# Optimization experiments

Measured on AMD Instinct MI355X. Metric: run time of the kernel, lower is better.

## Reference

```python
import jax, jax.numpy as jnp
import numpy as np
from jax import lax

B, T, DIN, D = 8, 4096, 1024, 256
H, DK, DV, DFF, P = 8, 32, 32, 1024, 4
KC, NS = 64, 4
SCALES = jnp.array([16.0, 64.0, 128.0, 256.0], dtype=jnp.float32)
K = KC * NS


def _pos_embedding(rel, d_model):
    # rel: [B,K,2] normalized (start,end) -> sinusoidal emb [B,K,d_model]
    d4 = d_model // 4
    freq = jnp.exp(-jnp.log(10000.0) * jnp.arange(d4, dtype=jnp.float32) / d4)
    ang = rel[..., None] * freq                                  # [B,K,2,d4]
    emb = jnp.concatenate([jnp.sin(ang), jnp.cos(ang)], axis=-1) # [B,K,2,2*d4]
    return emb.reshape(rel.shape[0], rel.shape[1], d_model)


def _pool(feat, s, e):
    # ROI pooling by P linearly spaced samples in [s,e); feat [B,T,D], s/e [B,K]
    frac = (jnp.arange(P, dtype=jnp.float32) + 0.5) / P
    idx = jnp.clip(jnp.floor(s[..., None] + (e - s)[..., None] * frac), 0, T - 1).astype(jnp.int32)
    b, k = idx.shape[0], idx.shape[1]
    out = jnp.take_along_axis(feat, idx.reshape(b, k * P)[..., None], axis=1)  # [B,K*P,D]
    return out.reshape(b, k, P, feat.shape[-1])


def _ln(x, g, b):
    m = x.mean(-1, keepdims=True)
    v = ((x - m) ** 2).mean(-1, keepdims=True)
    return (x - m) * lax.rsqrt(v + 1e-6) * g + b


def setup_inputs():
    ks = jax.random.split(jax.random.key(0), 16)
    n = lambda i, sh, s=0.02: jax.random.normal(ks[i], sh, jnp.float32) * s
    return dict(
        feature=jax.random.normal(ks[0], (B, T, DIN), jnp.float32),
        pos_ind=jnp.tile(jnp.arange(T, dtype=jnp.int32)[None], (B, 1)),
        feature_mask=jnp.ones((B, T), jnp.float32),
        W_red=n(1, (DIN, D)), b_red=jnp.zeros((D,), jnp.float32),
        conv1_w=n(2, (D, D, 3)), conv1_b=jnp.zeros((D,), jnp.float32),
        conv2_w=n(3, (D, D, 3)), conv2_b=jnp.zeros((D,), jnp.float32),
        W_sc=n(4, (D, 3)), b_sc=jnp.zeros((3,), jnp.float32),
        W_pool=n(5, (3 * P * D, D)), b_pool=jnp.zeros((D,), jnp.float32),
        Wq=n(6, (D, H * DK)), Wk=n(7, (D, H * DK)), Wv=n(8, (D, H * DV)),
        Wo=n(9, (H * DV, D)),
        ln1_g=jnp.ones((D,), jnp.float32), ln1_b=jnp.zeros((D,), jnp.float32),
        W1=n(10, (D, DFF)), b1=jnp.zeros((DFF,), jnp.float32),
        W2=n(11, (DFF, D)), b2=jnp.zeros((D,), jnp.float32),
        ln2_g=jnp.ones((D,), jnp.float32), ln2_b=jnp.zeros((D,), jnp.float32),
        W_cls=n(12, (D, 2)), b_cls=jnp.zeros((2,), jnp.float32),
    )


def _forward(feature, feature_mask, W_red, b_red, conv1_w, conv1_b, conv2_w, conv2_b,
             W_sc, b_sc, W_pool, b_pool, Wq, Wk, Wv, Wo, ln1_g, ln1_b,
             W1, b1, W2, b2, ln2_g, ln2_b, W_cls, b_cls):
    enc_input = jax.nn.selu(feature @ W_red + b_red)            # [B,T,D]
    h = enc_input.transpose(0, 2, 1)                            # [B,D,T]
    dn = ('NCH', 'OIH', 'NCH')
    h = jax.nn.relu(lax.conv_general_dilated(h, conv1_w, (1,), [(1, 1)], dimension_numbers=dn) + conv1_b[None, :, None])
    h = jax.nn.relu(lax.conv_general_dilated(h, conv2_w, (1,), [(1, 1)], dimension_numbers=dn) + conv2_b[None, :, None])
    enc_output = h.transpose(0, 2, 1)                           # [B,T,D]
    score_output = jax.nn.sigmoid(enc_output @ W_sc + b_sc)     # [B,T,3]

    # --- proposal_layer (fixed-size, jit-safe): top-KC actness peaks x NS scales ---
    actness = score_output[..., 0] * feature_mask               # [B,T]
    topv, topi = lax.top_k(actness, KC)                         # [B,KC]
    c = topi.astype(jnp.float32)[:, :, None]                    # [B,KC,1]
    half = SCALES[None, None, :] / 2.0
    s = jnp.clip(c - half, 0.0, T - 1.0).reshape(B, K)
    e = jnp.clip(c + half, 1.0, float(T)).reshape(B, K)
    e = jnp.maximum(e, s + 1.0)
    L = e - s
    ss, se = jnp.clip(s - L / 4, 0.0, T - 1.0), s + L / 4       # start region
    es, ee = e - L / 4, jnp.clip(e + L / 4, 1.0, float(T))      # end region
    rois_mask = jnp.broadcast_to((topv > 0.5)[:, :, None], (B, KC, NS)).reshape(B, K).astype(jnp.float32)
    roi_actness = jnp.broadcast_to(topv[:, :, None], (B, KC, NS)).reshape(B, K)
    rel = jnp.stack([s / T, e / T], axis=-1)                    # [B,K,2]
    pos_emb = _pos_embedding(rel, D)                            # [B,K,D]

    # --- ROI_Relation: pool(start/mid/end) -> fc -> MHSA + FFN (post-LN) ---
    pooled = jnp.concatenate([_pool(enc_input, ss, se), _pool(enc_input, s, e), _pool(enc_input, es, ee)], axis=2)
    x0 = pooled.reshape(B, K, 3 * P * D) @ W_pool + b_pool + pos_emb  # [B,K,D]
    q = (x0 @ Wq).reshape(B, K, H, DK)
    kk = (x0 @ Wk).reshape(B, K, H, DK)
    v = (x0 @ Wv).reshape(B, K, H, DV)
    att = jnp.einsum('bqhd,bkhd->bhqk', q, kk) / np.sqrt(DK).astype(np.float32)
    att = att + (1.0 - rois_mask)[:, None, None, :] * -1e9
    ctx = jnp.einsum('bhqk,bkhd->bqhd', jax.nn.softmax(att, axis=-1), v).reshape(B, K, H * DV)
    x1 = _ln(x0 + ctx @ Wo, ln1_g, ln1_b)
    x2 = _ln(x1 + jax.nn.relu(x1 @ W1 + b1) @ W2 + b2, ln2_g, ln2_b)
    roi_scores = jax.nn.softmax(x2 @ W_cls + b_cls, axis=2)     # [B,K,2]
    rois_se = jnp.stack([s, e], axis=-1)                        # rois[:, :, 1:]
    return rois_se, roi_actness, roi_scores


def reference(feature, pos_ind, feature_mask, W_red, b_red, conv1_w, conv1_b, conv2_w, conv2_b, W_sc, b_sc, W_pool, b_pool, Wq, Wk, Wv, Wo, ln1_g, ln1_b, W1, b1, W2, b2, ln2_g, ln2_b, W_cls, b_cls):
    del pos_ind  # carried through pipeline but unused in this forward
    return _forward(feature, feature_mask, W_red, b_red, conv1_w, conv1_b, conv2_w, conv2_b, W_sc, b_sc, W_pool, b_pool, Wq, Wk, Wv, Wo, ln1_g, ln1_b, W1, b1, W2, b2, ln2_g, ln2_b, W_cls, b_cls)
```

## Files before the change

kernel.cpp:

```cpp
#include <hip/hip_runtime.h>
#include <hip/hip_bf16.h>
#include <math.h>

#define NB 8
#define NT 4096
#define NBT 32768
#define NDIN 1024
#define ND 256
#define NH 8
#define NDK 32
#define NKC 64
#define NNS 4
#define NRK 256
#define NROI 2048

#define F4Z make_float4(0.f, 0.f, 0.f, 0.f)

__global__ __launch_bounds__(256) void transw_k(const float* __restrict__ w1,
    const float* __restrict__ w2, float* __restrict__ Wt1, float* __restrict__ Wt2)
{
  int i = blockIdx.x * 256 + threadIdx.x;
  const float* w = (i >= 196608) ? w2 : w1;
  float* Wt = (i >= 196608) ? Wt2 : Wt1;
  int j = (i >= 196608) ? (i - 196608) : i;
  int co = j & 255;
  int rest = j >> 8;
  int ci = rest & 255;
  int tap = rest >> 8;
  Wt[j] = w[(size_t)co * 768 + ci * 3 + tap];
}

__global__ __launch_bounds__(256) void concatw_k(const float* __restrict__ Wq,
    const float* __restrict__ Wk, const float* __restrict__ Wv,
    float* __restrict__ Wqkv)
{
  int d = blockIdx.x * 256 + threadIdx.x;
  int r = d / 768, c = d % 768;
  int m = c >> 8, cc = c & 255;
  const float* src = (m == 0) ? Wq : (m == 1) ? Wk : Wv;
  Wqkv[d] = src[r * 256 + cc];
}

__global__ __launch_bounds__(256) void gemm1_k(const float* __restrict__ A,
    const float* __restrict__ W, const float* __restrict__ bias,
    float* __restrict__ C, int M, int Ka, int N)
{
  __shared__ float As[16][132];
  __shared__ float Ws[16][128];
  int tid = threadIdx.x;
  int tx = tid & 15, ty = tid >> 4;
  int m0 = blockIdx.x * 128, n0 = blockIdx.y * 128;
  int ar = tid >> 1, acg = tid & 1;
  int wk = tid >> 5, wn = tid & 31;
  float4 pa0, pa1, pw0, pw1;

#define G1LOAD(kk) do { \
    pa0 = *reinterpret_cast<const float4*>(A + (size_t)(m0 + ar) * Ka + (kk) + (acg * 2 + 0) * 4); \
    pa1 = *reinterpret_cast<const float4*>(A + (size_t)(m0 + ar) * Ka + (kk) + (acg * 2 + 1) * 4); \
    pw0 = *reinterpret_cast<const float4*>(W + (size_t)((kk) + wk) * N + n0 + wn * 4); \
    pw1 = *reinterpret_cast<const float4*>(W + (size_t)((kk) + 8 + wk) * N + n0 + wn * 4); \
  } while (0)
#define G1WRITE() do { \
    int cg0 = acg * 2, cg1 = acg * 2 + 1; \
    As[cg0 * 4 + 0][ar] = pa0.x; As[cg0 * 4 + 1][ar] = pa0.y; \
    As[cg0 * 4 + 2][ar] = pa0.z; As[cg0 * 4 + 3][ar] = pa0.w; \
    As[cg1 * 4 + 0][ar] = pa1.x; As[cg1 * 4 + 1][ar] = pa1.y; \
    As[cg1 * 4 + 2][ar] = pa1.z; As[cg1 * 4 + 3][ar] = pa1.w; \
    *reinterpret_cast<float4*>(&Ws[wk][wn * 4]) = pw0; \
    *reinterpret_cast<float4*>(&Ws[8 + wk][wn * 4]) = pw1; \
  } while (0)

  int NC = Ka >> 4;
  float acc[8][8] = {};
  G1LOAD(0);
  G1WRITE();
  __syncthreads();
  for (int c = 0; c < NC; ++c) {
    if (c + 1 < NC) G1LOAD((c + 1) * 16);
#pragma unroll
    for (int k = 0; k < 16; ++k) {
      float4 xa = *reinterpret_cast<const float4*>(&As[k][ty * 4]);
      float4 xb = *reinterpret_cast<const float4*>(&As[k][64 + ty * 4]);
      float4 wa = *reinterpret_cast<const float4*>(&Ws[k][tx * 4]);
      float4 wb = *reinterpret_cast<const float4*>(&Ws[k][64 + tx * 4]);
      float aa[8] = {xa.x, xa.y, xa.z, xa.w, xb.x, xb.y, xb.z, xb.w};
      float bb[8] = {wa.x, wa.y, wa.z, wa.w, wb.x, wb.y, wb.z, wb.w};
#pragma unroll
      for (int i = 0; i < 8; ++i)
#pragma unroll
        for (int j = 0; j < 8; ++j)
          acc[i][j] += aa[i] * bb[j];
    }
    __syncthreads();
    if (c + 1 < NC) {
      G1WRITE();
      __syncthreads();
    }
  }
#undef G1LOAD
#undef G1WRITE
#pragma unroll
  for (int i = 0; i < 8; ++i) {
    int row = m0 + ((i < 4) ? (ty * 4 + i) : (64 + ty * 4 + (i - 4)));
#pragma unroll
    for (int jh = 0; jh < 2; ++jh) {
      int col = n0 + jh * 64 + tx * 4;
      float o[4];
#pragma unroll
      for (int j = 0; j < 4; ++j) {
        float v = acc[i][jh * 4 + j] + bias[col + j];
        v = (v > 0.f) ? 1.0507009873554805f * v
                      : 1.0507009873554805f * 1.6732632423543772f * expm1f(v);
        o[j] = v;
      }
      *reinterpret_cast<float4*>(C + (size_t)row * N + col) =
          make_float4(o[0], o[1], o[2], o[3]);
    }
  }
}

template<int EPI>
__global__ __launch_bounds__(256) void conv_t(const float* __restrict__ in,
    const float* __restrict__ Wt, const float* __restrict__ bias,
    float* __restrict__ out, const float* __restrict__ Wsc,
    float* __restrict__ pscore)
{
  __shared__ float As[16][132];
  __shared__ float Ws[16][128];
  int tid = threadIdx.x;
  int tx = tid & 15, ty = tid >> 4;
  int m0 = blockIdx.x * 128, n0 = blockIdx.y * 128;
  int bstart = m0 & ~(NT - 1);
  int ar = tid >> 1, acg = tid & 1;
  int wk = tid >> 5, wn = tid & 31;
  float4 pa0, pa1, pw0, pw1;

#define CLOAD(kk) do { \
    int tap = (kk) >> 8, kd = (kk) & 255; \
    int g = m0 - 1 + tap + ar; \
    bool ok = (g >= bstart) && (g < bstart + NT); \
    pa0 = ok ? *reinterpret_cast<const float4*>(in + (size_t)g * 256 + kd + (acg * 2 + 0) * 4) : F4Z; \
    pa1 = ok ? *reinterpret_cast<const float4*>(in + (size_t)g * 256 + kd + (acg * 2 + 1) * 4) : F4Z; \
    pw0 = *reinterpret_cast<const float4*>(Wt + (size_t)((kk) + wk) * 256 + n0 + wn * 4); \
    pw1 = *reinterpret_cast<const float4*>(Wt + (size_t)((kk) + 8 + wk) * 256 + n0 + wn * 4); \
  } while (0)
#define CWRITE() do { \
    int cg0 = acg * 2, cg1 = acg * 2 + 1; \
    As[cg0 * 4 + 0][ar] = pa0.x; As[cg0 * 4 + 1][ar] = pa0.y; \
    As[cg0 * 4 + 2][ar] = pa0.z; As[cg0 * 4 + 3][ar] = pa0.w; \
    As[cg1 * 4 + 0][ar] = pa1.x; As[cg1 * 4 + 1][ar] = pa1.y; \
    As[cg1 * 4 + 2][ar] = pa1.z; As[cg1 * 4 + 3][ar] = pa1.w; \
    *reinterpret_cast<float4*>(&Ws[wk][wn * 4]) = pw0; \
    *reinterpret_cast<float4*>(&Ws[8 + wk][wn * 4]) = pw1; \
  } while (0)

  float acc[8][8] = {};
  CLOAD(0);
  CWRITE();
  __syncthreads();
  for (int c = 0; c < 48; ++c) {
    if (c + 1 < 48) CLOAD((c + 1) * 16);
#pragma unroll
    for (int k = 0; k < 16; ++k) {
      float4 xa = *reinterpret_cast<const float4*>(&As[k][ty * 4]);
      float4 xb = *reinterpret_cast<const float4*>(&As[k][64 + ty * 4]);
      float4 wa = *reinterpret_cast<const float4*>(&Ws[k][tx * 4]);
      float4 wb = *reinterpret_cast<const float4*>(&Ws[k][64 + tx * 4]);
      float aa[8] = {xa.x, xa.y, xa.z, xa.w, xb.x, xb.y, xb.z, xb.w};
      float bb[8] = {wa.x, wa.y, wa.z, wa.w, wb.x, wb.y, wb.z, wb.w};
#pragma unroll
      for (int i = 0; i < 8; ++i)
#pragma unroll
        for (int j = 0; j < 8; ++j)
          acc[i][j] += aa[i] * bb[j];
    }
    __syncthreads();
    if (c + 1 < 48) {
      CWRITE();
      __syncthreads();
    }
  }
#undef CLOAD
#undef CWRITE

  if (EPI == 0) {
#pragma unroll
    for (int i = 0; i < 8; ++i) {
      int row = m0 + ((i < 4) ? (ty * 4 + i) : (64 + ty * 4 + (i - 4)));
#pragma unroll
      for (int jh = 0; jh < 2; ++jh) {
        int col = n0 + jh * 64 + tx * 4;
        float o[4];
#pragma unroll
        for (int j = 0; j < 4; ++j)
          o[j] = fmaxf(acc[i][jh * 4 + j] + bias[col + j], 0.f);
        *reinterpret_cast<float4*>(out + (size_t)row * 256 + col) =
            make_float4(o[0], o[1], o[2], o[3]);
      }
    }
  } else {
    float p[8];
#pragma unroll
    for (int i = 0; i < 8; ++i) {
      float s = 0.f;
#pragma unroll
      for (int jh = 0; jh < 2; ++jh)
#pragma unroll
        for (int j = 0; j < 4; ++j) {
          int col = n0 + jh * 64 + tx * 4 + j;
          float v = fmaxf(acc[i][jh * 4 + j] + bias[col], 0.f);
          s += v * Wsc[col * 3];
        }
      p[i] = s;
    }
#pragma unroll
    for (int off = 1; off < 16; off <<= 1)
#pragma unroll
      for (int i = 0; i < 8; ++i)
        p[i] += __shfl_xor(p[i], off, 64);
    if (tx == 0) {
#pragma unroll
      for (int i = 0; i < 8; ++i) {
        int row = m0 + ((i < 4) ? (ty * 4 + i) : (64 + ty * 4 + (i - 4)));
        pscore[(size_t)row * 2 + blockIdx.y] = p[i];
      }
    }
  }
}

__global__ __launch_bounds__(256) void actness_k(const float* __restrict__ pscore,
    const float* __restrict__ bsc, const float* __restrict__ fmask,
    float* __restrict__ actness)
{
  int g = blockIdx.x * 256 + threadIdx.x;
  float2 pv = *reinterpret_cast<const float2*>(pscore + (size_t)g * 2);
  float z = pv.x + pv.y + bsc[0];
  actness[g] = (1.f / (1.f + expf(-z))) * fmask[g];
}

template<int ACT>
__global__ __launch_bounds__(256) void gemm_k(const float* __restrict__ A,
    const float* __restrict__ W, const float* __restrict__ bias,
    const float* __restrict__ resid, float* __restrict__ C,
    int M, int Ka, int N)
{
  __shared__ float As[16][66];
  __shared__ float Ws[16][68];
  int tid = threadIdx.x;
  int tx = tid & 15, ty = tid >> 4;
  int m0 = blockIdx.x * 64, n0 = blockIdx.y * 64;
  int lr = tid >> 2, lc = tid & 3;
  int wr = tid >> 4, wc = tid & 15;
  float4 pav, pwv;
  int NC = Ka >> 4;

#define GLOAD(kk) do { \
    pav = *reinterpret_cast<const float4*>(A + (size_t)(m0 + lr) * Ka + (kk) + lc * 4); \
    pwv = *reinterpret_cast<const float4*>(W + (size_t)((kk) + wr) * N + n0 + wc * 4); \
  } while (0)
#define GWRITE() do { \
    As[lc * 4 + 0][lr] = pav.x; As[lc * 4 + 1][lr] = pav.y; \
    As[lc * 4 + 2][lr] = pav.z; As[lc * 4 + 3][lr] = pav.w; \
    *reinterpret_cast<float4*>(&Ws[wr][wc * 4]) = pwv; \
  } while (0)

  float acc[4][4] = {};
  GLOAD(0);
  GWRITE();
  __syncthreads();
  for (int c = 0; c < NC; ++c) {
    if (c + 1 < NC) GLOAD((c + 1) * 16);
#pragma unroll
    for (int k = 0; k < 16; ++k) {
      float4 a4 = *reinterpret_cast<const float4*>(&As[k][ty * 4]);
      float4 b4 = *reinterpret_cast<const float4*>(&Ws[k][tx * 4]);
      float aa[4] = {a4.x, a4.y, a4.z, a4.w};
      float bb[4] = {b4.x, b4.y, b4.z, b4.w};
#pragma unroll
      for (int i = 0; i < 4; ++i)
#pragma unroll
        for (int j = 0; j < 4; ++j)
          acc[i][j] += aa[i] * bb[j];
    }
    __syncthreads();
    if (c + 1 < NC) {
      GWRITE();
      __syncthreads();
    }
  }
#undef GLOAD
#undef GWRITE
#pragma unroll
  for (int i = 0; i < 4; ++i) {
    int row = m0 + ty * 4 + i;
    float o[4];
#pragma unroll
    for (int j = 0; j < 4; ++j) {
      int col = n0 + tx * 4 + j;
      float v = acc[i][j];
      if (bias) v += bias[col];
      if (resid) v += resid[(size_t)row * N + col];
      if (ACT == 1) {
        v = (v > 0.f) ? 1.0507009873554805f * v
                      : 1.0507009873554805f * 1.6732632423543772f * expm1f(v);
      } else if (ACT == 2) {
        v = fmaxf(v, 0.f);
      }
      o[j] = v;
    }
    *reinterpret_cast<float4*>(C + (size_t)row * N + n0 + tx * 4) =
        make_float4(o[0], o[1], o[2], o[3]);
  }
}

__global__ __launch_bounds__(256) void topk_k(const float* __restrict__ actness,
    float* __restrict__ topv, int* __restrict__ topi)
{
  __shared__ float wbv[4];
  __shared__ int wbi[4];
  __shared__ float gbv;
  __shared__ int gbi;
  int b = blockIdx.x;
  int tid = threadIdx.x;
  int lane = tid & 63, wvi = tid >> 6;
  float v[16];
  const float* src = actness + (size_t)b * NT + tid * 16;
#pragma unroll
  for (int j = 0; j < 16; j += 4)
    *reinterpret_cast<float4*>(&v[j]) = *reinterpret_cast<const float4*>(src + j);
  for (int it = 0; it < NKC; ++it) {
    float best = -1e30f; int bj = 0;
#pragma unroll
    for (int j = 0; j < 16; ++j)
      if (v[j] > best) { best = v[j]; bj = j; }
    int bidx = tid * 16 + bj;
#pragma unroll
    for (int off = 1; off < 64; off <<= 1) {
      float ov = __shfl_xor(best, off, 64);
      int oi = __shfl_xor(bidx, off, 64);
      if (ov > best || (ov == best && oi < bidx)) { best = ov; bidx = oi; }
    }
    if (lane == 0) { wbv[wvi] = best; wbi[wvi] = bidx; }
    __syncthreads();
    if (tid == 0) {
      float bb = wbv[0]; int bi2 = wbi[0];
#pragma unroll
      for (int w = 1; w < 4; ++w)
        if (wbv[w] > bb || (wbv[w] == bb && wbi[w] < bi2)) { bb = wbv[w]; bi2 = wbi[w]; }
      topv[b * NKC + it] = bb;
      topi[b * NKC + it] = bi2;
      gbv = bb; gbi = bi2;
    }
    __syncthreads();
    int gi = gbi;
    if ((gi >> 4) == tid) v[gi & 15] = -1e30f;
  }
}

__global__ __launch_bounds__(256) void rois_k(const float* __restrict__ topv,
    const int* __restrict__ topi, int* __restrict__ idxb, float* __restrict__ rmask,
    float* __restrict__ rel, float* __restrict__ out_rois, float* __restrict__ out_act)
{
  int t = blockIdx.x * 256 + threadIdx.x;
  if (t >= NROI) return;
  int b = t >> 8, k = t & 255, kc = k >> 2, ns = k & 3;
  float tv = topv[b * NKC + kc];
  float c = (float)topi[b * NKC + kc];
  const float scales[4] = {16.f, 64.f, 128.f, 256.f};
  float half = scales[ns] * 0.5f;
  float s = fminf(fmaxf(c - half, 0.f), 4095.f);
  float e = fminf(fmaxf(c + half, 1.f), 4096.f);
  e = fmaxf(e, s + 1.f);
  float L = e - s;
  float ss = fminf(fmaxf(s - L * 0.25f, 0.f), 4095.f);
  float se = s + L * 0.25f;
  float es = e - L * 0.25f;
  float ee = fminf(fmaxf(e + L * 0.25f, 1.f), 4096.f);
  float st[3] = {ss, s, es};
  float en[3] = {se, e, ee};
#pragma unroll
  for (int r = 0; r < 3; ++r)
#pragma unroll
    for (int p = 0; p < 4; ++p) {
      float frac = ((float)p + 0.5f) * 0.25f;
      float fidx = floorf(st[r] + (en[r] - st[r]) * frac);
      fidx = fminf(fmaxf(fidx, 0.f), 4095.f);
      idxb[t * 12 + r * 4 + p] = (int)fidx;
    }
  rmask[t] = (tv > 0.5f) ? 1.f : 0.f;
  rel[t * 2 + 0] = s * (1.f / 4096.f);
  rel[t * 2 + 1] = e * (1.f / 4096.f);
  out_rois[t * 2 + 0] = s;
  out_rois[t * 2 + 1] = e;
  out_act[t] = tv;
}

__global__ __launch_bounds__(256) void pool_gemm_k(const float* __restrict__ enc,
    const int* __restrict__ idxb, const float* __restrict__ Wp,
    const float* __restrict__ bp, const float* __restrict__ rel,
    float* __restrict__ x0)
{
  __shared__ float As[16][66];
  __shared__ float Ws[16][68];
  int tid = threadIdx.x;
  int tx = tid & 15, ty = tid >> 4;
  int m0 = blockIdx.x * 64, n0 = blockIdx.y * 64;
  int lr = tid >> 2, lc = tid & 3;
  int wr = tid >> 4, wc = tid & 15;
  int roi = m0 + lr;
  int b = roi >> 8;
  float4 pav, pwv;

#define PLOAD(kk) do { \
    int slot = (kk) >> 8, kd = (kk) & 255; \
    int trow = idxb[roi * 12 + slot]; \
    pav = *reinterpret_cast<const float4*>(enc + ((size_t)(b * NT + trow)) * 256 + kd + lc * 4); \
    pwv = *reinterpret_cast<const float4*>(Wp + (size_t)((kk) + wr) * 256 + n0 + wc * 4); \
  } while (0)
#define PWRITE() do { \
    As[lc * 4 + 0][lr] = pav.x; As[lc * 4 + 1][lr] = pav.y; \
    As[lc * 4 + 2][lr] = pav.z; As[lc * 4 + 3][lr] = pav.w; \
    *reinterpret_cast<float4*>(&Ws[wr][wc * 4]) = pwv; \
  } while (0)

  float acc[4][4] = {};
  PLOAD(0);
  PWRITE();
  __syncthreads();
  for (int c = 0; c < 192; ++c) {
    if (c + 1 < 192) PLOAD((c + 1) * 16);
#pragma unroll
    for (int k = 0; k < 16; ++k) {
      float4 a4 = *reinterpret_cast<const float4*>(&As[k][ty * 4]);
      float4 b4 = *reinterpret_cast<const float4*>(&Ws[k][tx * 4]);
      float aa[4] = {a4.x, a4.y, a4.z, a4.w};
      float bb[4] = {b4.x, b4.y, b4.z, b4.w};
#pragma unroll
      for (int i = 0; i < 4; ++i)
#pragma unroll
        for (int j = 0; j < 4; ++j)
          acc[i][j] += aa[i] * bb[j];
    }
    __syncthreads();
    if (c + 1 < 192) {
      PWRITE();
      __syncthreads();
    }
  }
#undef PLOAD
#undef PWRITE
#pragma unroll
  for (int i = 0; i < 4; ++i) {
    int rr = m0 + ty * 4 + i;
    float r0 = rel[rr * 2], r1 = rel[rr * 2 + 1];
    float o[4];
#pragma unroll
    for (int j = 0; j < 4; ++j) {
      int col = n0 + tx * 4 + j;
      int rsel = col >> 7, cc = col & 127, j2 = cc & 63;
      float freq = expf(-0.14391156831212787f * (float)j2);
      float ang = ((rsel == 0) ? r0 : r1) * freq;
      float pe = (cc < 64) ? sinf(ang) : cosf(ang);
      o[j] = acc[i][j] + bp[col] + pe;
    }
    *reinterpret_cast<float4*>(x0 + (size_t)rr * 256 + n0 + tx * 4) =
        make_float4(o[0], o[1], o[2], o[3]);
  }
}

__global__ __launch_bounds__(256) void attn_k(const float* __restrict__ qkv,
    const float* __restrict__ rmask, float* __restrict__ ctx)
{
  __shared__ float ks[256][32];
  __shared__ float vs[256][32];
  int bh = blockIdx.x;
  int b = bh >> 3, h = bh & 7;
  int tid = threadIdx.x;
  size_t rowb = (size_t)b * 256;
  for (int idx = tid; idx < 2048; idx += 256) {
    int r = idx >> 3, dg = idx & 7;
    *reinterpret_cast<float4*>(&ks[r][dg * 4]) =
        *reinterpret_cast<const float4*>(qkv + (rowb + r) * 768 + 256 + h * 32 + dg * 4);
    *reinterpret_cast<float4*>(&vs[r][dg * 4]) =
        *reinterpret_cast<const float4*>(qkv + (rowb + r) * 768 + 512 + h * 32 + dg * 4);
  }
  __syncthreads();
  float qr[32];
#pragma unroll
  for (int dg = 0; dg < 8; ++dg)
    *reinterpret_cast<float4*>(&qr[dg * 4]) =
        *reinterpret_cast<const float4*>(qkv + (rowb + tid) * 768 + h * 32 + dg * 4);
  const float invs = 0.17677669529663689f;
  float m = -1e30f, l = 0.f;
  float accd[32] = {};
  for (int kk = 0; kk < 256; ++kk) {
    float s = 0.f;
#pragma unroll
    for (int d = 0; d < 32; ++d) s += qr[d] * ks[kk][d];
    s = s * invs + (1.f - rmask[b * 256 + kk]) * -1e9f;
    if (s > m) {
      float corr = expf(m - s);
      l *= corr;
#pragma unroll
      for (int d = 0; d < 32; ++d) accd[d] *= corr;
      m = s;
    }
    float p = expf(s - m);
    l += p;
#pragma unroll
    for (int d = 0; d < 32; ++d) accd[d] += p * vs[kk][d];
  }
  float inv = 1.f / l;
#pragma unroll
  for (int dg = 0; dg < 8; ++dg) {
    float4 o = make_float4(accd[dg * 4] * inv, accd[dg * 4 + 1] * inv,
                           accd[dg * 4 + 2] * inv, accd[dg * 4 + 3] * inv);
    *reinterpret_cast<float4*>(ctx + (rowb + tid) * 256 + h * 32 + dg * 4) = o;
  }
}

__global__ __launch_bounds__(256) void ln_k(float* __restrict__ x,
    const float* __restrict__ g, const float* __restrict__ bb)
{
  int row = blockIdx.x * 4 + (threadIdx.x >> 6);
  int lane = threadIdx.x & 63;
  float* xr = x + (size_t)row * 256;
  float4 v = *reinterpret_cast<const float4*>(xr + lane * 4);
  float s = v.x + v.y + v.z + v.w;
#pragma unroll
  for (int off = 32; off > 0; off >>= 1) s += __shfl_xor(s, off, 64);
  float mean = s * 0.00390625f;
  float dx[4] = {v.x - mean, v.y - mean, v.z - mean, v.w - mean};
  float s2 = dx[0] * dx[0] + dx[1] * dx[1] + dx[2] * dx[2] + dx[3] * dx[3];
#pragma unroll
  for (int off = 32; off > 0; off >>= 1) s2 += __shfl_xor(s2, off, 64);
  float var = s2 * 0.00390625f;
  float rs = 1.f / sqrtf(var + 1e-6f);
  int c = lane * 4;
  float4 o;
  o.x = dx[0] * rs * g[c + 0] + bb[c + 0];
  o.y = dx[1] * rs * g[c + 1] + bb[c + 1];
  o.z = dx[2] * rs * g[c + 2] + bb[c + 2];
  o.w = dx[3] * rs * g[c + 3] + bb[c + 3];
  *reinterpret_cast<float4*>(xr + lane * 4) = o;
}

__global__ __launch_bounds__(256) void cls_k(const float* __restrict__ x2,
    const float* __restrict__ Wc, const float* __restrict__ bc,
    float* __restrict__ out)
{
  int row = blockIdx.x * 4 + (threadIdx.x >> 6);
  int lane = threadIdx.x & 63;
  const float* xr = x2 + (size_t)row * 256;
  float4 xv = *reinterpret_cast<const float4*>(xr + lane * 4);
  int c = lane * 4;
  float4 w01 = *reinterpret_cast<const float4*>(Wc + c * 2);
  float4 w23 = *reinterpret_cast<const float4*>(Wc + c * 2 + 4);
  float l0 = xv.x * w01.x + xv.y * w01.z + xv.z * w23.x + xv.w * w23.z;
  float l1 = xv.x * w01.y + xv.y * w01.w + xv.z * w23.y + xv.w * w23.w;
#pragma unroll
  for (int off = 32; off > 0; off >>= 1) {
    l0 += __shfl_xor(l0, off, 64);
    l1 += __shfl_xor(l1, off, 64);
  }
  if (lane == 0) {
    l0 += bc[0]; l1 += bc[1];
    float mm = fmaxf(l0, l1);
    float e0 = expf(l0 - mm), e1 = expf(l1 - mm);
    float inv = 1.f / (e0 + e1);
    out[row * 2 + 0] = e0 * inv;
    out[row * 2 + 1] = e1 * inv;
  }
}

extern "C" void kernel_launch(void* const* d_in, const int* in_sizes, int n_in,
                              void* d_out, int out_size, void* d_ws, size_t ws_size,
                              hipStream_t stream) {
  (void)in_sizes; (void)n_in; (void)out_size; (void)ws_size;
  const float* feature = (const float*)d_in[0];
  const float* fmask   = (const float*)d_in[2];
  const float* W_red   = (const float*)d_in[3];
  const float* b_red   = (const float*)d_in[4];
  const float* conv1_w = (const float*)d_in[5];
  const float* conv1_b = (const float*)d_in[6];
  const float* conv2_w = (const float*)d_in[7];
  const float* conv2_b = (const float*)d_in[8];
  const float* W_sc    = (const float*)d_in[9];
  const float* b_sc    = (const float*)d_in[10];
  const float* W_pool  = (const float*)d_in[11];
  const float* b_pool  = (const float*)d_in[12];
  const float* Wq      = (const float*)d_in[13];
  const float* Wk      = (const float*)d_in[14];
  const float* Wv      = (const float*)d_in[15];
  const float* Wo      = (const float*)d_in[16];
  const float* ln1_g   = (const float*)d_in[17];
  const float* ln1_b   = (const float*)d_in[18];
  const float* W1      = (const float*)d_in[19];
  const float* b1      = (const float*)d_in[20];
  const float* W2      = (const float*)d_in[21];
  const float* b2      = (const float*)d_in[22];
  const float* ln2_g   = (const float*)d_in[23];
  const float* ln2_b   = (const float*)d_in[24];
  const float* W_cls   = (const float*)d_in[25];
  const float* b_cls   = (const float*)d_in[26];

  float* ws = (float*)d_ws;
  float* enc   = ws;
  float* h1    = ws + 8388608;
  float* Wt1   = ws + 16777216;
  float* Wt2   = ws + 16973824;
  float* act   = ws + 17170432;
  float* topv  = ws + 17203200;
  int*   topi  = (int*)(ws + 17203712);
  int*   idxb  = (int*)(ws + 17204224);
  float* rmask = ws + 17228800;
  float* rel   = ws + 17230848;
  float* pscore = ws + 17234944;
  float* x0   = h1;
  float* qkv  = h1 + 524288;
  float* ctx  = h1 + 2097152;
  float* x1   = h1 + 2621440;
  float* ft   = h1 + 3145728;
  float* x2   = h1 + 5242880;
  float* Wqkv = h1 + 5767168;

  float* orois  = (float*)d_out;
  float* oact   = orois + 4096;
  float* oscore = orois + 6144;

  transw_k<<<1536, 256, 0, stream>>>(conv1_w, conv2_w, Wt1, Wt2);
  gemm1_k<<<dim3(256, 2), 256, 0, stream>>>(feature, W_red, b_red, enc,
                                            NBT, NDIN, ND);
  conv_t<0><<<dim3(256, 2), 256, 0, stream>>>(enc, Wt1, conv1_b, h1, nullptr, nullptr);
  conv_t<1><<<dim3(256, 2), 256, 0, stream>>>(h1, Wt2, conv2_b, nullptr, W_sc, pscore);
  actness_k<<<128, 256, 0, stream>>>(pscore, b_sc, fmask, act);
  topk_k<<<NB, 256, 0, stream>>>(act, topv, topi);
  rois_k<<<NB, 256, 0, stream>>>(topv, topi, idxb, rmask, rel, orois, oact);
  concatw_k<<<768, 256, 0, stream>>>(Wq, Wk, Wv, Wqkv);
  pool_gemm_k<<<dim3(32, 4), 256, 0, stream>>>(enc, idxb, W_pool, b_pool, rel, x0);
  gemm_k<0><<<dim3(32, 12), 256, 0, stream>>>(x0, Wqkv, nullptr, nullptr, qkv,
                                              NROI, ND, 768);
  attn_k<<<NB * NH, 256, 0, stream>>>(qkv, rmask, ctx);
  gemm_k<0><<<dim3(32, 4), 256, 0, stream>>>(ctx, Wo, nullptr, x0, x1, NROI, ND, ND);
  ln_k<<<512, 256, 0, stream>>>(x1, ln1_g, ln1_b);
  gemm_k<2><<<dim3(32, 16), 256, 0, stream>>>(x1, W1, b1, nullptr, ft, NROI, ND, 1024);
  gemm_k<0><<<dim3(32, 4), 256, 0, stream>>>(ft, W2, b2, x1, x2, NROI, 1024, ND);
  ln_k<<<512, 256, 0, stream>>>(x2, ln2_g, ln2_b);
  cls_k<<<512, 256, 0, stream>>>(x2, W_cls, b_cls, oscore);
}
```

Measured before the change: 1.197 ms.

## Enlarge GEMM/conv tiles to 256 rows with 512 threads; drop prefetch in small GEMMs

The main GEMM and both conv kernels now use 512-thread blocks covering 256 rows by 128 columns, so each weight tile staged in shared memory serves twice as many rows and the grid is halved. Each thread still computes an 8x8 output fragment. Separately, the small gemm_k and pool_gemm_k kernels drop their register prefetch double-buffering in favour of a simpler load-sync-compute loop, which lowers register pressure but exposes global load latency. The larger blocks increase shared memory and register use per block, which may reduce occupancy.

```diff
diff --git a/kernel.cpp b/kernel.cpp
--- a/kernel.cpp
+++ b/kernel.cpp
@@ -41,24 +41,23 @@
   Wqkv[d] = src[r * 256 + cc];
 }
 
-__global__ __launch_bounds__(256) void gemm1_k(const float* __restrict__ A,
+__global__ __launch_bounds__(512) void gemm1_k(const float* __restrict__ A,
     const float* __restrict__ W, const float* __restrict__ bias,
     float* __restrict__ C, int M, int Ka, int N)
 {
-  __shared__ float As[16][132];
+  __shared__ float As[16][264];
   __shared__ float Ws[16][128];
   int tid = threadIdx.x;
   int tx = tid & 15, ty = tid >> 4;
-  int m0 = blockIdx.x * 128, n0 = blockIdx.y * 128;
+  int m0 = blockIdx.x * 256, n0 = blockIdx.y * 128;
   int ar = tid >> 1, acg = tid & 1;
   int wk = tid >> 5, wn = tid & 31;
-  float4 pa0, pa1, pw0, pw1;
+  float4 pa0, pa1, pw0;
 
 #define G1LOAD(kk) do { \
     pa0 = *reinterpret_cast<const float4*>(A + (size_t)(m0 + ar) * Ka + (kk) + (acg * 2 + 0) * 4); \
     pa1 = *reinterpret_cast<const float4*>(A + (size_t)(m0 + ar) * Ka + (kk) + (acg * 2 + 1) * 4); \
     pw0 = *reinterpret_cast<const float4*>(W + (size_t)((kk) + wk) * N + n0 + wn * 4); \
-    pw1 = *reinterpret_cast<const float4*>(W + (size_t)((kk) + 8 + wk) * N + n0 + wn * 4); \
   } while (0)
 #define G1WRITE() do { \
     int cg0 = acg * 2, cg1 = acg * 2 + 1; \
@@ -67,7 +66,6 @@
     As[cg1 * 4 + 0][ar] = pa1.x; As[cg1 * 4 + 1][ar] = pa1.y; \
     As[cg1 * 4 + 2][ar] = pa1.z; As[cg1 * 4 + 3][ar] = pa1.w; \
     *reinterpret_cast<float4*>(&Ws[wk][wn * 4]) = pw0; \
-    *reinterpret_cast<float4*>(&Ws[8 + wk][wn * 4]) = pw1; \
   } while (0)
 
   int NC = Ka >> 4;
@@ -80,7 +78,7 @@
 #pragma unroll
     for (int k = 0; k < 16; ++k) {
       float4 xa = *reinterpret_cast<const float4*>(&As[k][ty * 4]);
-      float4 xb = *reinterpret_cast<const float4*>(&As[k][64 + ty * 4]);
+      float4 xb = *reinterpret_cast<const float4*>(&As[k][128 + ty * 4]);
       float4 wa = *reinterpret_cast<const float4*>(&Ws[k][tx * 4]);
       float4 wb = *reinterpret_cast<const float4*>(&Ws[k][64 + tx * 4]);
       float aa[8] = {xa.x, xa.y, xa.z, xa.w, xb.x, xb.y, xb.z, xb.w};
@@ -101,7 +99,7 @@
 #undef G1WRITE
 #pragma unroll
   for (int i = 0; i < 8; ++i) {
-    int row = m0 + ((i < 4) ? (ty * 4 + i) : (64 + ty * 4 + (i - 4)));
+    int row = m0 + ((i < 4) ? (ty * 4 + i) : (128 + ty * 4 + (i - 4)));
 #pragma unroll
     for (int jh = 0; jh < 2; ++jh) {
       int col = n0 + jh * 64 + tx * 4;
@@ -120,20 +118,20 @@
 }
 
 template<int EPI>
-__global__ __launch_bounds__(256) void conv_t(const float* __restrict__ in,
+__global__ __launch_bounds__(512) void conv_t(const float* __restrict__ in,
     const float* __restrict__ Wt, const float* __restrict__ bias,
     float* __restrict__ out, const float* __restrict__ Wsc,
     float* __restrict__ pscore)
 {
-  __shared__ float As[16][132];
+  __shared__ float As[16][264];
   __shared__ float Ws[16][128];
   int tid = threadIdx.x;
   int tx = tid & 15, ty = tid >> 4;
-  int m0 = blockIdx.x * 128, n0 = blockIdx.y * 128;
+  int m0 = blockIdx.x * 256, n0 = blockIdx.y * 128;
   int bstart = m0 & ~(NT - 1);
   int ar = tid >> 1, acg = tid & 1;
   int wk = tid >> 5, wn = tid & 31;
-  float4 pa0, pa1, pw0, pw1;
+  float4 pa0, pa1, pw0;
 
 #define CLOAD(kk) do { \
     int tap = (kk) >> 8, kd = (kk) & 255; \
@@ -142,7 +140,6 @@
     pa0 = ok ? *reinterpret_cast<const float4*>(in + (size_t)g * 256 + kd + (acg * 2 + 0) * 4) : F4Z; \
     pa1 = ok ? *reinterpret_cast<const float4*>(in + (size_t)g * 256 + kd + (acg * 2 + 1) * 4) : F4Z; \
     pw0 = *reinterpret_cast<const float4*>(Wt + (size_t)((kk) + wk) * 256 + n0 + wn * 4); \
-    pw1 = *reinterpret_cast<const float4*>(Wt + (size_t)((kk) + 8 + wk) * 256 + n0 + wn * 4); \
   } while (0)
 #define CWRITE() do { \
     int cg0 = acg * 2, cg1 = acg * 2 + 1; \
@@ -151,7 +148,6 @@
     As[cg1 * 4 + 0][ar] = pa1.x; As[cg1 * 4 + 1][ar] = pa1.y; \
     As[cg1 * 4 + 2][ar] = pa1.z; As[cg1 * 4 + 3][ar] = pa1.w; \
     *reinterpret_cast<float4*>(&Ws[wk][wn * 4]) = pw0; \
-    *reinterpret_cast<float4*>(&Ws[8 + wk][wn * 4]) = pw1; \
   } while (0)
 
   float acc[8][8] = {};
@@ -163,7 +159,7 @@
 #pragma unroll
     for (int k = 0; k < 16; ++k) {
       float4 xa = *reinterpret_cast<const float4*>(&As[k][ty * 4]);
-      float4 xb = *reinterpret_cast<const float4*>(&As[k][64 + ty * 4]);
+      float4 xb = *reinterpret_cast<const float4*>(&As[k][128 + ty * 4]);
       float4 wa = *reinterpret_cast<const float4*>(&Ws[k][tx * 4]);
       float4 wb = *reinterpret_cast<const float4*>(&Ws[k][64 + tx * 4]);
       float aa[8] = {xa.x, xa.y, xa.z, xa.w, xb.x, xb.y, xb.z, xb.w};
@@ -186,7 +182,7 @@
   if (EPI == 0) {
 #pragma unroll
     for (int i = 0; i < 8; ++i) {
-      int row = m0 + ((i < 4) ? (ty * 4 + i) : (64 + ty * 4 + (i - 4)));
+      int row = m0 + ((i < 4) ? (ty * 4 + i) : (128 + ty * 4 + (i - 4)));
 #pragma unroll
       for (int jh = 0; jh < 2; ++jh) {
         int col = n0 + jh * 64 + tx * 4;
@@ -221,7 +217,7 @@
     if (tx == 0) {
 #pragma unroll
       for (int i = 0; i < 8; ++i) {
-        int row = m0 + ((i < 4) ? (ty * 4 + i) : (64 + ty * 4 + (i - 4)));
+        int row = m0 + ((i < 4) ? (ty * 4 + i) : (128 + ty * 4 + (i - 4)));
         pscore[(size_t)row * 2 + blockIdx.y] = p[i];
       }
     }
@@ -251,25 +247,16 @@
   int m0 = blockIdx.x * 64, n0 = blockIdx.y * 64;
   int lr = tid >> 2, lc = tid & 3;
   int wr = tid >> 4, wc = tid & 15;
-  float4 pav, pwv;
-  int NC = Ka >> 4;
-
-#define GLOAD(kk) do { \
-    pav = *reinterpret_cast<const float4*>(A + (size_t)(m0 + lr) * Ka + (kk) + lc * 4); \
-    pwv = *reinterpret_cast<const float4*>(W + (size_t)((kk) + wr) * N + n0 + wc * 4); \
-  } while (0)
-#define GWRITE() do { \
-    As[lc * 4 + 0][lr] = pav.x; As[lc * 4 + 1][lr] = pav.y; \
-    As[lc * 4 + 2][lr] = pav.z; As[lc * 4 + 3][lr] = pav.w; \
-    *reinterpret_cast<float4*>(&Ws[wr][wc * 4]) = pwv; \
-  } while (0)
-
   float acc[4][4] = {};
-  GLOAD(0);
-  GWRITE();
-  __syncthreads();
-  for (int c = 0; c < NC; ++c) {
-    if (c + 1 < NC) GLOAD((c + 1) * 16);
+  for (int kk = 0; kk < Ka; kk += 16) {
+    float4 av = *reinterpret_cast<const float4*>(A + (size_t)(m0 + lr) * Ka + kk + lc * 4);
+    As[lc * 4 + 0][lr] = av.x;
+    As[lc * 4 + 1][lr] = av.y;
+    As[lc * 4 + 2][lr] = av.z;
+    As[lc * 4 + 3][lr] = av.w;
+    float4 wv = *reinterpret_cast<const float4*>(W + (size_t)(kk + wr) * N + n0 + wc * 4);
+    *reinterpret_cast<float4*>(&Ws[wr][wc * 4]) = wv;
+    __syncthreads();
 #pragma unroll
     for (int k = 0; k < 16; ++k) {
       float4 a4 = *reinterpret_cast<const float4*>(&As[k][ty * 4]);
@@ -283,13 +270,7 @@
           acc[i][j] += aa[i] * bb[j];
     }
     __syncthreads();
-    if (c + 1 < NC) {
-      GWRITE();
-      __syncthreads();
-    }
-  }
-#undef GLOAD
-#undef GWRITE
+  }
 #pragma unroll
   for (int i = 0; i < 4; ++i) {
     int row = m0 + ty * 4 + i;
@@ -409,26 +390,19 @@
   int wr = tid >> 4, wc = tid & 15;
   int roi = m0 + lr;
   int b = roi >> 8;
-  float4 pav, pwv;
-
-#define PLOAD(kk) do { \
-    int slot = (kk) >> 8, kd = (kk) & 255; \
-    int trow = idxb[roi * 12 + slot]; \
-    pav = *reinterpret_cast<const float4*>(enc + ((size_t)(b * NT + trow)) * 256 + kd + lc * 4); \
-    pwv = *reinterpret_cast<const float4*>(Wp + (size_t)((kk) + wr) * 256 + n0 + wc * 4); \
-  } while (0)
-#define PWRITE() do { \
-    As[lc * 4 + 0][lr] = pav.x; As[lc * 4 + 1][lr] = pav.y; \
-    As[lc * 4 + 2][lr] = pav.z; As[lc * 4 + 3][lr] = pav.w; \
-    *reinterpret_cast<float4*>(&Ws[wr][wc * 4]) = pwv; \
-  } while (0)
-
   float acc[4][4] = {};
-  PLOAD(0);
-  PWRITE();
-  __syncthreads();
-  for (int c = 0; c < 192; ++c) {
-    if (c + 1 < 192) PLOAD((c + 1) * 16);
+  for (int kk = 0; kk < 3072; kk += 16) {
+    int slot = kk >> 8, kd = kk & 255;
+    int trow = idxb[roi * 12 + slot];
+    float4 av = *reinterpret_cast<const float4*>(
+        enc + ((size_t)(b * NT + trow)) * 256 + kd + lc * 4);
+    As[lc * 4 + 0][lr] = av.x;
+    As[lc * 4 + 1][lr] = av.y;
+    As[lc * 4 + 2][lr] = av.z;
+    As[lc * 4 + 3][lr] = av.w;
+    float4 wv = *reinterpret_cast<const float4*>(Wp + (size_t)(kk + wr) * 256 + n0 + wc * 4);
+    *reinterpret_cast<float4*>(&Ws[wr][wc * 4]) = wv;
+    __syncthreads();
 #pragma unroll
     for (int k = 0; k < 16; ++k) {
       float4 a4 = *reinterpret_cast<const float4*>(&As[k][ty * 4]);
@@ -442,13 +416,7 @@
           acc[i][j] += aa[i] * bb[j];
     }
     __syncthreads();
-    if (c + 1 < 192) {
-      PWRITE();
-      __syncthreads();
-    }
-  }
-#undef PLOAD
-#undef PWRITE
+  }
 #pragma unroll
   for (int i = 0; i < 4; ++i) {
     int rr = m0 + ty * 4 + i;
@@ -629,10 +597,10 @@
   float* oscore = orois + 6144;
 
   transw_k<<<1536, 256, 0, stream>>>(conv1_w, conv2_w, Wt1, Wt2);
-  gemm1_k<<<dim3(256, 2), 256, 0, stream>>>(feature, W_red, b_red, enc,
+  gemm1_k<<<dim3(128, 2), 512, 0, stream>>>(feature, W_red, b_red, enc,
                                             NBT, NDIN, ND);
-  conv_t<0><<<dim3(256, 2), 256, 0, stream>>>(enc, Wt1, conv1_b, h1, nullptr, nullptr);
-  conv_t<1><<<dim3(256, 2), 256, 0, stream>>>(h1, Wt2, conv2_b, nullptr, W_sc, pscore);
+  conv_t<0><<<dim3(128, 2), 512, 0, stream>>>(enc, Wt1, conv1_b, h1, nullptr, nullptr);
+  conv_t<1><<<dim3(128, 2), 512, 0, stream>>>(h1, Wt2, conv2_b, nullptr, W_sc, pscore);
   actness_k<<<128, 256, 0, stream>>>(pscore, b_sc, fmask, act);
   topk_k<<<NB, 256, 0, stream>>>(act, topv, topi);
   rois_k<<<NB, 256, 0, stream>>>(topv, topi, idxb, rmask, rel, orois, oact);
```

Result: slower. 3.316 ms (+177.0%).
